# Performance work log

Hardware: AMD Instinct MI355X
Metric: run time of the kernel (lower is better)

## Reference

```python
import jax, jax.numpy as jnp
import numpy as np

HID, H, P = 1024, 16, 50  # hid_dim, n_heads, max_relative_position
DH = HID // H


def _rel_idx(len_q, len_k):
    # [Lq, Lk] clipped relative-distance indices into the (2P+1)-row table
    d = jnp.arange(len_k)[None, :] - jnp.arange(len_q)[:, None]
    return jnp.clip(d, -P, P) + P


def setup_inputs() -> dict:
    key = jax.random.key(0)
    ks = jax.random.split(key, 13)
    L, B = 2048, 2
    s = 0.02
    return {
        "query": jax.random.normal(ks[0], (L, B, HID), jnp.float32),
        "key": jax.random.normal(ks[1], (L, B, HID), jnp.float32),
        "value": jax.random.normal(ks[2], (L, B, HID), jnp.float32),
        "Wq": jax.random.normal(ks[3], (HID, HID), jnp.float32) * s,
        "bq": jax.random.normal(ks[4], (HID,), jnp.float32) * s,
        "Wk": jax.random.normal(ks[5], (HID, HID), jnp.float32) * s,
        "bk": jax.random.normal(ks[6], (HID,), jnp.float32) * s,
        "Wv": jax.random.normal(ks[7], (HID, HID), jnp.float32) * s,
        "bv": jax.random.normal(ks[8], (HID,), jnp.float32) * s,
        "Wo": jax.random.normal(ks[9], (HID, HID), jnp.float32) * s,
        "bo": jax.random.normal(ks[10], (HID,), jnp.float32) * s,
        "rel_k": jax.random.normal(ks[11], (2 * P + 1, DH), jnp.float32) * s,
        "rel_v": jax.random.normal(ks[12], (2 * P + 1, DH), jnp.float32) * s,
    }


def reference(query, key, value, Wq, bq, Wk, bk, Wv, bv, Wo, bo, rel_k, rel_v):
    # inputs are seq-first [L, B, hid]; torch code transposes to batch-first
    q = jnp.swapaxes(query, 0, 1)  # [B, Lq, hid]
    k = jnp.swapaxes(key, 0, 1)
    v = jnp.swapaxes(value, 0, 1)
    B, Lq, _ = q.shape
    Lk = k.shape[1]

    q = q @ Wq.T + bq
    k = k @ Wk.T + bk
    v = v @ Wv.T + bv

    # split heads: [B, H, L, DH]
    qh = q.reshape(B, Lq, H, DH).transpose(0, 2, 1, 3)
    kh = k.reshape(B, Lk, H, DH).transpose(0, 2, 1, 3)
    vh = v.reshape(B, Lk, H, DH).transpose(0, 2, 1, 3)

    idx = _rel_idx(Lq, Lk)
    Rk = rel_k[idx]  # [Lq, Lk, DH]
    Rv = rel_v[idx]  # [Lq, Lk, DH]

    attn1 = jnp.einsum('bhqd,bhkd->bhqk', qh, kh)
    attn2 = jnp.einsum('bhqd,qkd->bhqk', qh, Rk)
    scale = jnp.asarray(np.sqrt(DH), qh.dtype)
    attn = jax.nn.softmax((attn1 + attn2) / scale, axis=-1)  # dropout p=0 -> identity

    w1 = jnp.einsum('bhqk,bhkd->bhqd', attn, vh)
    w2 = jnp.einsum('bhqk,qkd->bhqd', attn, Rv)
    x = (w1 + w2).transpose(0, 2, 1, 3).reshape(B, Lq, HID)
    x = x @ Wo.T + bo
    return jnp.swapaxes(x, 0, 1)  # [Lq, B, hid]
```

## Files before the change

kernel.cpp:

```cpp
#include <hip/hip_runtime.h>


#define LSEQ 2048
#define HIDDIM 1024
#define NH 16
#define DHD 64
#define NREL 101
#define PMAX 50
#define SCL 0.18033688011112042f

typedef __attribute__((ext_vector_type(8))) __bf16 bf16x8;
typedef __attribute__((ext_vector_type(4))) float f32x4;

__device__ __forceinline__ unsigned short f2bf(float f) {
  unsigned int u = __builtin_bit_cast(unsigned int, f);
  u += 0x7fffu + ((u >> 16) & 1u);
  return (unsigned short)(u >> 16);
}
__device__ __forceinline__ float bflo(unsigned int u) { return __builtin_bit_cast(float, u << 16); }

__device__ __forceinline__ uint4 pack8(float4 f0, float4 f1) {
  uint4 o;
  o.x = (unsigned)f2bf(f0.x) | ((unsigned)f2bf(f0.y) << 16);
  o.y = (unsigned)f2bf(f0.z) | ((unsigned)f2bf(f0.w) << 16);
  o.z = (unsigned)f2bf(f1.x) | ((unsigned)f2bf(f1.y) << 16);
  o.w = (unsigned)f2bf(f1.z) | ((unsigned)f2bf(f1.w) << 16);
  return o;
}

__global__ void cast_w4(const float* __restrict__ s0, const float* __restrict__ s1,
                        const float* __restrict__ s2, const float* __restrict__ s3,
                        unsigned short* __restrict__ dst) {
  const int e = (blockIdx.x * 256 + threadIdx.x) * 8;
  const int g = e >> 20;
  const float* s = (g == 0) ? s0 : (g == 1) ? s1 : (g == 2) ? s2 : s3;
  const int o = e & 0xFFFFF;
  const float4 f0 = *(const float4*)(s + o);
  const float4 f1 = *(const float4*)(s + o + 4);
  *(uint4*)(dst + e) = pack8(f0, f1);
}

__global__ void cast_x_kernel(const float* __restrict__ src, unsigned short* __restrict__ dst) {
  const int e = (blockIdx.x * 256 + threadIdx.x) * 8;
  const int m = e >> 10, k = e & 1023;
  const int b = m >> 11, l = m & 2047;
  const float* s = src + (size_t)((l << 1) + b) * HIDDIM + k;
  const float4 f0 = *(const float4*)s;
  const float4 f1 = *(const float4*)(s + 4);
  *(uint4*)(dst + e) = pack8(f0, f1);
}

__global__ void cast_rk_kernel(const float* __restrict__ src, unsigned short* __restrict__ dst) {
  const int e = blockIdx.x * 256 + threadIdx.x;
  if (e >= 112 * 64) return;
  dst[e] = (e < NREL * 64) ? f2bf(src[e]) : (unsigned short)0;
}

__global__ void cast_rv_kernel(const float* __restrict__ src, unsigned short* __restrict__ dst) {
  const int e = blockIdx.x * 256 + threadIdx.x;
  if (e >= 64 * 128) return;
  const int d = e >> 7, j = e & 127;
  dst[e] = (j < NREL) ? f2bf(src[j * DHD + d]) : (unsigned short)0;
}

template <int MODE>
__global__ __launch_bounds__(256, 4) void gemm64(
    const unsigned short* __restrict__ A,
    const unsigned short* __restrict__ W,
    const float* __restrict__ bias,
    float* __restrict__ outF,
    unsigned short* __restrict__ outB) {
  constexpr int K = 1024;
  __shared__ unsigned short As[64 * 72];
  __shared__ unsigned short Bs[64 * 72];
  const int tid = threadIdx.x;
  const int tm = blockIdx.x >> 4, tn = blockIdx.x & 15;
  const int m0 = tm * 64, n0 = tn * 64;
  const int lane = tid & 63, wave = tid >> 6;
  const int wm = (wave >> 1) * 32, wn = (wave & 1) * 32;
  const int qr = lane & 15, quad = lane >> 4;
  const int sr = tid >> 3, sc = (tid & 7) * 8;
  f32x4 acc[2][2] = {};
  for (int k0 = 0; k0 < K; k0 += 64) {
    *(uint4*)&As[sr * 72 + sc]        = *(const uint4*)&A[(size_t)(m0 + sr) * K + k0 + sc];
    *(uint4*)&As[(sr + 32) * 72 + sc] = *(const uint4*)&A[(size_t)(m0 + sr + 32) * K + k0 + sc];
    *(uint4*)&Bs[sr * 72 + sc]        = *(const uint4*)&W[(size_t)(n0 + sr) * K + k0 + sc];
    *(uint4*)&Bs[(sr + 32) * 72 + sc] = *(const uint4*)&W[(size_t)(n0 + sr + 32) * K + k0 + sc];
    __syncthreads();
#pragma unroll
    for (int ks = 0; ks < 64; ks += 32) {
      bf16x8 a0 = *(const bf16x8*)&As[(wm + qr) * 72 + ks + quad * 8];
      bf16x8 a1 = *(const bf16x8*)&As[(wm + 16 + qr) * 72 + ks + quad * 8];
      bf16x8 b0 = *(const bf16x8*)&Bs[(wn + qr) * 72 + ks + quad * 8];
      bf16x8 b1 = *(const bf16x8*)&Bs[(wn + 16 + qr) * 72 + ks + quad * 8];
      acc[0][0] = __builtin_amdgcn_mfma_f32_16x16x32_bf16(a0, b0, acc[0][0], 0, 0, 0);
      acc[0][1] = __builtin_amdgcn_mfma_f32_16x16x32_bf16(a0, b1, acc[0][1], 0, 0, 0);
      acc[1][0] = __builtin_amdgcn_mfma_f32_16x16x32_bf16(a1, b0, acc[1][0], 0, 0, 0);
      acc[1][1] = __builtin_amdgcn_mfma_f32_16x16x32_bf16(a1, b1, acc[1][1], 0, 0, 0);
    }
    __syncthreads();
  }
#pragma unroll
  for (int i = 0; i < 2; i++)
#pragma unroll
    for (int j = 0; j < 2; j++) {
      const int n = n0 + wn + 16 * j + qr;
      const float bv = bias[n];
#pragma unroll
      for (int rr = 0; rr < 4; rr++) {
        const int m = m0 + wm + 16 * i + quad * 4 + rr;
        const float v = acc[i][j][rr] + bv;
        const int b = m >> 11, l = m & 2047;
        if (MODE == 0) {
          const int h = n >> 6, d = n & 63;
          outB[((size_t)((b * NH + h) * LSEQ + l) << 6) + d] = f2bf(v);
        } else if (MODE == 1) {
          outF[(size_t)((l << 1) + b) * HIDDIM + n] = v;
        } else {
          const int h = n >> 6, d = n & 63;
          outB[(size_t)((b * NH + h) * 64 + d) * LSEQ + l] = f2bf(v);
        }
      }
    }
}

#define KT 32
__global__ __launch_bounds__(256, 4) void attn_mfma(
    const unsigned short* __restrict__ Qb,
    const unsigned short* __restrict__ Kb,
    const unsigned short* __restrict__ Vgt,
    const unsigned short* __restrict__ RKb,
    const unsigned short* __restrict__ RVb,
    unsigned short* __restrict__ outB) {
  __shared__ __align__(16) unsigned short SH[20416];
  unsigned short* Kst = SH;
  unsigned short* Tb  = SH + 7424;
  unsigned short* SrS = SH + 13952;

  const int tid = threadIdx.x;
  const int xcd = blockIdx.x & 7, slot = blockIdx.x >> 3;
  const int bh = (slot >> 5) * 8 + xcd;
  const int q0 = (slot & 31) * 64;

  const int lane = tid & 63, wq = tid >> 6;
  const int c = lane & 15, quad = lane >> 4;
  const size_t base = (size_t)bh * (LSEQ * DHD);
  const unsigned short* Qp = Qb + base;
  const unsigned short* Kp = Kb + base;
  const unsigned short* Vp = Vgt + base;
  unsigned short* Ptw = SH + 4608 + wq * 704;

  const int qrow_w = q0 + wq * 16;
  const int srow = quad * 4;
  const int wrow0 = wq * 16 + srow;

  {
    unsigned* tz = (unsigned*)(Tb + wq * 1632);
    for (int e = lane; e < 816; e += 64) tz[e] = 0u;
  }

  const bf16x8 aq0 = *(const bf16x8*)&Qp[(size_t)(qrow_w + c) * DHD + quad * 8];
  const bf16x8 aq1 = *(const bf16x8*)&Qp[(size_t)(qrow_w + c) * DHD + 32 + quad * 8];

#pragma unroll
  for (int jt = 0; jt < 7; jt++) {
    bf16x8 b0 = *(const bf16x8*)&RKb[(jt * 16 + c) * DHD + quad * 8];
    bf16x8 b1 = *(const bf16x8*)&RKb[(jt * 16 + c) * DHD + 32 + quad * 8];
    f32x4 s4 = {};
    s4 = __builtin_amdgcn_mfma_f32_16x16x32_bf16(aq0, b0, s4, 0, 0, 0);
    s4 = __builtin_amdgcn_mfma_f32_16x16x32_bf16(aq1, b1, s4, 0, 0, 0);
    const int jc = jt * 16 + c;
    if (jc < NREL) {
#pragma unroll
      for (int r = 0; r < 4; r++) SrS[(wrow0 + r) * NREL + jc] = f2bf(s4[r]);
    }
  }

  float Srlo[4], Srhi[4];
#pragma unroll
  for (int r = 0; r < 4; r++) {
    Srlo[r] = bflo((unsigned)SrS[(wrow0 + r) * NREL + 0]);
    Srhi[r] = bflo((unsigned)SrS[(wrow0 + r) * NREL + 100]);
  }

  float rsum[4] = {0.f, 0.f, 0.f, 0.f};
  float lows[4] = {0.f, 0.f, 0.f, 0.f}, highs[4] = {0.f, 0.f, 0.f, 0.f};
  f32x4 Od[4] = {};

  const int strow = tid >> 3, stcol = (tid & 7) * 8;

  {
    uint4 k0r = *(const uint4*)&Kp[(size_t)strow * DHD + stcol];
    *(uint4*)&Kst[strow * 72 + stcol] = k0r;
  }
  __syncthreads();

  for (int it = 0; it < 64; ++it) {
    const int k0 = it * KT;
    const int cur = (it & 1) * 2304;
    uint4 kreg;
    if (it < 63) kreg = *(const uint4*)&Kp[(size_t)(k0 + KT + strow) * DHD + stcol];
    bf16x8 vf[4];
#pragma unroll
    for (int t = 0; t < 4; t++)
      vf[t] = *(const bf16x8*)&Vp[(size_t)(t * 16 + c) * LSEQ + k0 + quad * 8];

    const bf16x8 bk00 = *(const bf16x8*)&Kst[cur + c * 72 + quad * 8];
    const bf16x8 bk01 = *(const bf16x8*)&Kst[cur + c * 72 + 32 + quad * 8];
    const bf16x8 bk10 = *(const bf16x8*)&Kst[cur + (16 + c) * 72 + quad * 8];
    const bf16x8 bk11 = *(const bf16x8*)&Kst[cur + (16 + c) * 72 + 32 + quad * 8];
    f32x4 s0 = {}, s1 = {};
    s0 = __builtin_amdgcn_mfma_f32_16x16x32_bf16(aq0, bk00, s0, 0, 0, 0);
    s0 = __builtin_amdgcn_mfma_f32_16x16x32_bf16(aq1, bk01, s0, 0, 0, 0);
    s1 = __builtin_amdgcn_mfma_f32_16x16x32_bf16(aq0, bk10, s1, 0, 0, 0);
    s1 = __builtin_amdgcn_mfma_f32_16x16x32_bf16(aq1, bk11, s1, 0, 0, 0);

    const int mode = (k0 + KT - 1 <= qrow_w - 50) ? 0 : (k0 >= qrow_w + 65) ? 2 : 1;

#pragma unroll
    for (int kt = 0; kt < 2; kt++) {
      const f32x4 s = kt ? s1 : s0;
      const int kcol = k0 + kt * 16 + c;
#pragma unroll
      for (int r = 0; r < 4; r++) {
        float srv;
        int j = -1;
        if (mode == 0) srv = Srlo[r];
        else if (mode == 2) srv = Srhi[r];
        else {
          int dl = kcol - (qrow_w + srow + r);
          dl = dl < -PMAX ? -PMAX : (dl > PMAX ? PMAX : dl);
          j = dl + PMAX;
          srv = bflo((unsigned)SrS[(wrow0 + r) * NREL + j]);
        }
        const float p = exp2f((s[r] + srv) * SCL);
        const unsigned short pb = f2bf(p);
        const float pf = bflo((unsigned)pb);
        rsum[r] += pf;
        if (mode == 0) lows[r] += pf;
        else if (mode == 2) highs[r] += pf;
        else {
          if (j == 0) lows[r] += pf;
          else if (j == 100) highs[r] += pf;
          else Tb[(wrow0 + r) * 102 + j] = pb;
        }
        Ptw[(srow + r) * 44 + kt * 16 + c] = pb;
      }
    }

    const uint2 aplo = *(const uint2*)&Ptw[c * 44 + quad * 8];
    const uint2 aphi = *(const uint2*)&Ptw[c * 44 + quad * 8 + 4];
    const bf16x8 ap = __builtin_bit_cast(bf16x8, (uint4){aplo.x, aplo.y, aphi.x, aphi.y});
#pragma unroll
    for (int t = 0; t < 4; t++)
      Od[t] = __builtin_amdgcn_mfma_f32_16x16x32_bf16(ap, vf[t], Od[t], 0, 0, 0);

    if (it < 63) *(uint4*)&Kst[(cur ^ 2304) + strow * 72 + stcol] = kreg;
    __syncthreads();
  }

#pragma unroll
  for (int m = 1; m < 16; m <<= 1) {
#pragma unroll
    for (int r = 0; r < 4; r++) {
      rsum[r] += __shfl_xor(rsum[r], m, 64);
      lows[r] += __shfl_xor(lows[r], m, 64);
      highs[r] += __shfl_xor(highs[r], m, 64);
    }
  }
  if (c == 0) {
#pragma unroll
    for (int r = 0; r < 4; r++) {
      Tb[(wrow0 + r) * 102 + 0]   = f2bf(lows[r]);
      Tb[(wrow0 + r) * 102 + 100] = f2bf(highs[r]);
    }
  }
  __syncthreads();

#pragma unroll
  for (int kc = 0; kc < 4; kc++) {
    unsigned short a8[8];
#pragma unroll
    for (int jj = 0; jj < 8; jj++) {
      const int j = kc * 32 + quad * 8 + jj;
      a8[jj] = (j <= 100) ? Tb[(wq * 16 + c) * 102 + j] : (unsigned short)0;
    }
    bf16x8 at;
#pragma unroll
    for (int jj = 0; jj < 8; jj++) at[jj] = __builtin_bit_cast(__bf16, a8[jj]);
#pragma unroll
    for (int t = 0; t < 4; t++) {
      const bf16x8 bv = *(const bf16x8*)&RVb[(t * 16 + c) * 128 + kc * 32 + quad * 8];
      Od[t] = __builtin_amdgcn_mfma_f32_16x16x32_bf16(at, bv, Od[t], 0, 0, 0);
    }
  }

  const int b = bh >> 4, h = bh & 15;
#pragma unroll
  for (int r = 0; r < 4; r++) {
    const float inv = 1.f / rsum[r];
    const int qg = q0 + wq * 16 + srow + r;
    unsigned short* op = outB + (size_t)(b * LSEQ + qg) * HIDDIM + h * DHD + c;
#pragma unroll
    for (int t = 0; t < 4; t++) op[t * 16] = f2bf(Od[t][r] * inv);
  }
}

extern "C" void kernel_launch(void* const* d_in, const int* in_sizes, int n_in,
                              void* d_out, int out_size, void* d_ws, size_t ws_size,
                              hipStream_t stream) {
  const float* query = (const float*)d_in[0];
  const float* key   = (const float*)d_in[1];
  const float* value = (const float*)d_in[2];
  const float* Wq = (const float*)d_in[3];  const float* bq = (const float*)d_in[4];
  const float* Wk = (const float*)d_in[5];  const float* bk = (const float*)d_in[6];
  const float* Wv = (const float*)d_in[7];  const float* bv = (const float*)d_in[8];
  const float* Wo = (const float*)d_in[9];  const float* bo = (const float*)d_in[10];
  const float* relk = (const float*)d_in[11];
  const float* relv = (const float*)d_in[12];
  float* out = (float*)d_out;

  char* w = (char*)d_ws;
  const size_t MB = 1ull << 20;
  unsigned short* Wqb = (unsigned short*)(w + 0 * MB);
  unsigned short* Wkb = (unsigned short*)(w + 2 * MB);
  unsigned short* Wvb = (unsigned short*)(w + 4 * MB);
  unsigned short* Wob = (unsigned short*)(w + 6 * MB);
  unsigned short* Xb  = (unsigned short*)(w + 8 * MB);
  unsigned short* Qb  = (unsigned short*)(w + 16 * MB);
  unsigned short* Kb  = (unsigned short*)(w + 24 * MB);
  unsigned short* Vgt = (unsigned short*)(w + 32 * MB);
  unsigned short* AOb = Xb;
  unsigned short* RKb = Wqb;
  unsigned short* RVb = Wkb;

  cast_w4<<<2048, 256, 0, stream>>>(Wq, Wk, Wv, Wo, Wqb);

  cast_x_kernel<<<2048, 256, 0, stream>>>(query, Xb);
  gemm64<0><<<1024, 256, 0, stream>>>(Xb, Wqb, bq, nullptr, Qb);
  cast_rk_kernel<<<28, 256, 0, stream>>>(relk, RKb);
  cast_x_kernel<<<2048, 256, 0, stream>>>(key, Xb);
  gemm64<0><<<1024, 256, 0, stream>>>(Xb, Wkb, bk, nullptr, Kb);
  cast_rv_kernel<<<32, 256, 0, stream>>>(relv, RVb);
  cast_x_kernel<<<2048, 256, 0, stream>>>(value, Xb);
  gemm64<2><<<1024, 256, 0, stream>>>(Xb, Wvb, bv, nullptr, Vgt);

  attn_mfma<<<1024, 256, 0, stream>>>(Qb, Kb, Vgt, RKb, RVb, AOb);

  gemm64<1><<<1024, 256, 0, stream>>>(AOb, Wob, bo, out, nullptr);
}
```

Before: 390.5 us.

## Fuse QKV projections into one 128x128 GEMM with direct global-to-LDS loads

Replaces three separate cast-then-gemm64 sequences with a single cast kernel covering query/key/value and one batched QKV GEMM using 128x128 tiles, XOR-swizzled LDS, and global_load_lds transfers. The V output is transposed through shared memory so the Vgt stores are coalesced. The output buffer serves as scratch for the bf16 key and value inputs. This cuts launch count and redundant global traffic and raises per-block data reuse, at the cost of fewer blocks (768) and lower occupancy, plus a single-buffered load loop with no prefetch overlap.

```diff
diff --git a/kernel.cpp b/kernel.cpp
--- a/kernel.cpp
+++ b/kernel.cpp
@@ -12,6 +12,8 @@
 typedef __attribute__((ext_vector_type(8))) __bf16 bf16x8;
 typedef __attribute__((ext_vector_type(4))) float f32x4;
 
+#define MFMA(A, B, C) __builtin_amdgcn_mfma_f32_16x16x32_bf16(A, B, C, 0, 0, 0)
+
 __device__ __forceinline__ unsigned short f2bf(float f) {
   unsigned int u = __builtin_bit_cast(unsigned int, f);
   u += 0x7fffu + ((u >> 16) & 1u);
@@ -26,6 +28,12 @@
   o.z = (unsigned)f2bf(f1.x) | ((unsigned)f2bf(f1.y) << 16);
   o.w = (unsigned)f2bf(f1.z) | ((unsigned)f2bf(f1.w) << 16);
   return o;
+}
+
+__device__ __forceinline__ void gload16(const unsigned short* g, unsigned short* l) {
+  __builtin_amdgcn_global_load_lds(
+      (const __attribute__((address_space(1))) unsigned int*)g,
+      (__attribute__((address_space(3))) unsigned int*)l, 16, 0, 0);
 }
 
 __global__ void cast_w4(const float* __restrict__ s0, const float* __restrict__ s1,
@@ -40,13 +48,20 @@
   *(uint4*)(dst + e) = pack8(f0, f1);
 }
 
-__global__ void cast_x_kernel(const float* __restrict__ src, unsigned short* __restrict__ dst) {
-  const int e = (blockIdx.x * 256 + threadIdx.x) * 8;
-  const int m = e >> 10, k = e & 1023;
+__global__ void cast_x3(const float* __restrict__ q, const float* __restrict__ k,
+                        const float* __restrict__ v,
+                        unsigned short* __restrict__ dq, unsigned short* __restrict__ dk,
+                        unsigned short* __restrict__ dv) {
+  const int gid = blockIdx.x * 256 + threadIdx.x;
+  const int segi = gid >> 19;
+  const int e = (gid & 0x7FFFF) * 8;
+  const float* s = (segi == 0) ? q : (segi == 1) ? k : v;
+  unsigned short* dst = (segi == 0) ? dq : (segi == 1) ? dk : dv;
+  const int m = e >> 10, kk = e & 1023;
   const int b = m >> 11, l = m & 2047;
-  const float* s = src + (size_t)((l << 1) + b) * HIDDIM + k;
-  const float4 f0 = *(const float4*)s;
-  const float4 f1 = *(const float4*)(s + 4);
+  const float* sp = s + (size_t)((l << 1) + b) * HIDDIM + kk;
+  const float4 f0 = *(const float4*)sp;
+  const float4 f1 = *(const float4*)(sp + 4);
   *(uint4*)(dst + e) = pack8(f0, f1);
 }
 
@@ -61,6 +76,106 @@
   if (e >= 64 * 128) return;
   const int d = e >> 7, j = e & 127;
   dst[e] = (j < NREL) ? f2bf(src[j * DHD + d]) : (unsigned short)0;
+}
+
+__global__ __launch_bounds__(256, 3) void gemm_qkv(
+    const unsigned short* __restrict__ Xq, const unsigned short* __restrict__ Xk,
+    const unsigned short* __restrict__ Xv, const unsigned short* __restrict__ Wcat,
+    const float* __restrict__ bq, const float* __restrict__ bk, const float* __restrict__ bv,
+    unsigned short* __restrict__ Qb, unsigned short* __restrict__ Kb,
+    unsigned short* __restrict__ Vgt) {
+  __shared__ __align__(16) unsigned short SH[17408];
+  unsigned short* LA = SH;
+  unsigned short* LB = SH + 8192;
+
+  const int tid = threadIdx.x;
+  const int seg = blockIdx.x >> 8;
+  const int t = blockIdx.x & 255;
+  const int m0 = (t >> 3) * 128, n0 = (t & 7) * 128;
+
+  const unsigned short* A = (seg == 0) ? Xq : (seg == 1) ? Xk : Xv;
+  const unsigned short* W = Wcat + ((size_t)seg << 20);
+  const float* bias = (seg == 0) ? bq : (seg == 1) ? bk : bv;
+
+  const int lane = tid & 63, w = tid >> 6;
+  const int c = lane & 15, quad = lane >> 4;
+
+  const int srow = w * 32 + (lane >> 3);
+  const int scol = ((lane & 7) ^ (lane >> 3)) << 3;
+  const unsigned short* pA = A + (size_t)(m0 + srow) * 1024 + scol;
+  const unsigned short* pW = W + (size_t)(n0 + srow) * 1024 + scol;
+  unsigned short* lA = LA + w * 2048;
+  unsigned short* lB = LB + w * 2048;
+
+  const int wr = w >> 1, wc = w & 1;
+  const int cx = (c & 7) << 3;
+
+  f32x4 acc[4][4] = {};
+
+  for (int k0 = 0; k0 < 1024; k0 += 64) {
+#pragma unroll
+    for (int i = 0; i < 4; i++) {
+      gload16(pA + k0 + i * 8192, lA + i * 512);
+      gload16(pW + k0 + i * 8192, lB + i * 512);
+    }
+    __syncthreads();
+#pragma unroll
+    for (int ks = 0; ks < 2; ks++) {
+      bf16x8 af[4], bfr[4];
+#pragma unroll
+      for (int f = 0; f < 4; f++) {
+        af[f]  = *(const bf16x8*)&LA[(wr * 64 + f * 16 + c) * 64 + ((ks * 32 + quad * 8) ^ cx)];
+        bfr[f] = *(const bf16x8*)&LB[(wc * 64 + f * 16 + c) * 64 + ((ks * 32 + quad * 8) ^ cx)];
+      }
+#pragma unroll
+      for (int i = 0; i < 4; i++)
+#pragma unroll
+        for (int j = 0; j < 4; j++)
+          acc[i][j] = MFMA(af[i], bfr[j], acc[i][j]);
+    }
+    __syncthreads();
+  }
+
+  const int b = m0 >> 11, l0 = m0 & 2047;
+  const int h0 = n0 >> 6;
+  if (seg < 2) {
+    unsigned short* out = seg ? Kb : Qb;
+#pragma unroll
+    for (int i = 0; i < 4; i++)
+#pragma unroll
+      for (int j = 0; j < 4; j++) {
+        const int nl = wc * 64 + j * 16 + c;
+        const float bv_ = bias[n0 + nl];
+        const int h = h0 + (nl >> 6), d = nl & 63;
+#pragma unroll
+        for (int r = 0; r < 4; r++) {
+          const int l = l0 + wr * 64 + i * 16 + quad * 4 + r;
+          out[((size_t)((b * NH + h) * LSEQ + l) << 6) + d] = f2bf(acc[i][j][r] + bv_);
+        }
+      }
+  } else {
+    unsigned short* Ct = SH;
+#pragma unroll
+    for (int i = 0; i < 4; i++)
+#pragma unroll
+      for (int j = 0; j < 4; j++) {
+        const int nl = wc * 64 + j * 16 + c;
+        const float bv_ = bias[n0 + nl];
+#pragma unroll
+        for (int r = 0; r < 4; r++) {
+          const int ml = wr * 64 + i * 16 + quad * 4 + r;
+          Ct[nl * 136 + ml] = f2bf(acc[i][j][r] + bv_);
+        }
+      }
+    __syncthreads();
+    const int dr = tid >> 1, lc = (tid & 1) * 64;
+    const int h = h0 + (dr >> 6), dd = dr & 63;
+    unsigned short* dst = Vgt + ((size_t)((b * NH + h) * 64 + dd)) * LSEQ + l0 + lc;
+    const unsigned short* src = Ct + dr * 136 + lc;
+#pragma unroll
+    for (int u = 0; u < 8; u++)
+      *(uint4*)(dst + u * 8) = *(const uint4*)(src + u * 8);
+  }
 }
 
 template <int MODE>
@@ -93,10 +208,10 @@
       bf16x8 a1 = *(const bf16x8*)&As[(wm + 16 + qr) * 72 + ks + quad * 8];
       bf16x8 b0 = *(const bf16x8*)&Bs[(wn + qr) * 72 + ks + quad * 8];
       bf16x8 b1 = *(const bf16x8*)&Bs[(wn + 16 + qr) * 72 + ks + quad * 8];
-      acc[0][0] = __builtin_amdgcn_mfma_f32_16x16x32_bf16(a0, b0, acc[0][0], 0, 0, 0);
-      acc[0][1] = __builtin_amdgcn_mfma_f32_16x16x32_bf16(a0, b1, acc[0][1], 0, 0, 0);
-      acc[1][0] = __builtin_amdgcn_mfma_f32_16x16x32_bf16(a1, b0, acc[1][0], 0, 0, 0);
-      acc[1][1] = __builtin_amdgcn_mfma_f32_16x16x32_bf16(a1, b1, acc[1][1], 0, 0, 0);
+      acc[0][0] = MFMA(a0, b0, acc[0][0]);
+      acc[0][1] = MFMA(a0, b1, acc[0][1]);
+      acc[1][0] = MFMA(a1, b0, acc[1][0]);
+      acc[1][1] = MFMA(a1, b1, acc[1][1]);
     }
     __syncthreads();
   }
@@ -111,14 +226,8 @@
         const int m = m0 + wm + 16 * i + quad * 4 + rr;
         const float v = acc[i][j][rr] + bv;
         const int b = m >> 11, l = m & 2047;
-        if (MODE == 0) {
-          const int h = n >> 6, d = n & 63;
-          outB[((size_t)((b * NH + h) * LSEQ + l) << 6) + d] = f2bf(v);
-        } else if (MODE == 1) {
+        if (MODE == 1) {
           outF[(size_t)((l << 1) + b) * HIDDIM + n] = v;
-        } else {
-          const int h = n >> 6, d = n & 63;
-          outB[(size_t)((b * NH + h) * 64 + d) * LSEQ + l] = f2bf(v);
         }
       }
     }
@@ -167,8 +276,8 @@
     bf16x8 b0 = *(const bf16x8*)&RKb[(jt * 16 + c) * DHD + quad * 8];
     bf16x8 b1 = *(const bf16x8*)&RKb[(jt * 16 + c) * DHD + 32 + quad * 8];
     f32x4 s4 = {};
-    s4 = __builtin_amdgcn_mfma_f32_16x16x32_bf16(aq0, b0, s4, 0, 0, 0);
-    s4 = __builtin_amdgcn_mfma_f32_16x16x32_bf16(aq1, b1, s4, 0, 0, 0);
+    s4 = MFMA(aq0, b0, s4);
+    s4 = MFMA(aq1, b1, s4);
     const int jc = jt * 16 + c;
     if (jc < NREL) {
 #pragma unroll
@@ -210,10 +319,10 @@
     const bf16x8 bk10 = *(const bf16x8*)&Kst[cur + (16 + c) * 72 + quad * 8];
     const bf16x8 bk11 = *(const bf16x8*)&Kst[cur + (16 + c) * 72 + 32 + quad * 8];
     f32x4 s0 = {}, s1 = {};
-    s0 = __builtin_amdgcn_mfma_f32_16x16x32_bf16(aq0, bk00, s0, 0, 0, 0);
-    s0 = __builtin_amdgcn_mfma_f32_16x16x32_bf16(aq1, bk01, s0, 0, 0, 0);
-    s1 = __builtin_amdgcn_mfma_f32_16x16x32_bf16(aq0, bk10, s1, 0, 0, 0);
-    s1 = __builtin_amdgcn_mfma_f32_16x16x32_bf16(aq1, bk11, s1, 0, 0, 0);
+    s0 = MFMA(aq0, bk00, s0);
+    s0 = MFMA(aq1, bk01, s0);
+    s1 = MFMA(aq0, bk10, s1);
+    s1 = MFMA(aq1, bk11, s1);
 
     const int mode = (k0 + KT - 1 <= qrow_w - 50) ? 0 : (k0 >= qrow_w + 65) ? 2 : 1;
 
@@ -253,7 +362,7 @@
     const bf16x8 ap = __builtin_bit_cast(bf16x8, (uint4){aplo.x, aplo.y, aphi.x, aphi.y});
 #pragma unroll
     for (int t = 0; t < 4; t++)
-      Od[t] = __builtin_amdgcn_mfma_f32_16x16x32_bf16(ap, vf[t], Od[t], 0, 0, 0);
+      Od[t] = MFMA(ap, vf[t], Od[t]);
 
     if (it < 63) *(uint4*)&Kst[(cur ^ 2304) + strow * 72 + stcol] = kreg;
     __syncthreads();
@@ -291,7 +400,7 @@
 #pragma unroll
     for (int t = 0; t < 4; t++) {
       const bf16x8 bv = *(const bf16x8*)&RVb[(t * 16 + c) * 128 + kc * 32 + quad * 8];
-      Od[t] = __builtin_amdgcn_mfma_f32_16x16x32_bf16(at, bv, Od[t], 0, 0, 0);
+      Od[t] = MFMA(at, bv, Od[t]);
     }
   }
 
@@ -322,30 +431,23 @@
 
   char* w = (char*)d_ws;
   const size_t MB = 1ull << 20;
-  unsigned short* Wqb = (unsigned short*)(w + 0 * MB);
-  unsigned short* Wkb = (unsigned short*)(w + 2 * MB);
-  unsigned short* Wvb = (unsigned short*)(w + 4 * MB);
-  unsigned short* Wob = (unsigned short*)(w + 6 * MB);
-  unsigned short* Xb  = (unsigned short*)(w + 8 * MB);
-  unsigned short* Qb  = (unsigned short*)(w + 16 * MB);
-  unsigned short* Kb  = (unsigned short*)(w + 24 * MB);
-  unsigned short* Vgt = (unsigned short*)(w + 32 * MB);
-  unsigned short* AOb = Xb;
-  unsigned short* RKb = Wqb;
-  unsigned short* RVb = Wkb;
-
-  cast_w4<<<2048, 256, 0, stream>>>(Wq, Wk, Wv, Wo, Wqb);
-
-  cast_x_kernel<<<2048, 256, 0, stream>>>(query, Xb);
-  gemm64<0><<<1024, 256, 0, stream>>>(Xb, Wqb, bq, nullptr, Qb);
+  unsigned short* Wcat = (unsigned short*)(w + 0 * MB);
+  unsigned short* Wob  = (unsigned short*)(w + 6 * MB);
+  unsigned short* Xq   = (unsigned short*)(w + 8 * MB);
+  unsigned short* Qb   = (unsigned short*)(w + 16 * MB);
+  unsigned short* Kb   = (unsigned short*)(w + 24 * MB);
+  unsigned short* Vgt  = (unsigned short*)(w + 32 * MB);
+  unsigned short* AOb  = Xq;
+  unsigned short* RKb  = Wcat;
+  unsigned short* RVb  = (unsigned short*)(w + 2 * MB);
+  unsigned short* Xk = (unsigned short*)out;
+  unsigned short* Xv = (unsigned short*)out + (4u << 20);
+
+  cast_w4<<<2048, 256, 0, stream>>>(Wq, Wk, Wv, Wo, Wcat);
+  cast_x3<<<6144, 256, 0, stream>>>(query, key, value, Xq, Xk, Xv);
+  gemm_qkv<<<768, 256, 0, stream>>>(Xq, Xk, Xv, Wcat, bq, bk, bv, Qb, Kb, Vgt);
   cast_rk_kernel<<<28, 256, 0, stream>>>(relk, RKb);
-  cast_x_kernel<<<2048, 256, 0, stream>>>(key, Xb);
-  gemm64<0><<<1024, 256, 0, stream>>>(Xb, Wkb, bk, nullptr, Kb);
   cast_rv_kernel<<<32, 256, 0, stream>>>(relv, RVb);
-  cast_x_kernel<<<2048, 256, 0, stream>>>(value, Xb);
-  gemm64<2><<<1024, 256, 0, stream>>>(Xb, Wvb, bv, nullptr, Vgt);
-
   attn_mfma<<<1024, 256, 0, stream>>>(Qb, Kb, Vgt, RKb, RVb, AOb);
-
   gemm64<1><<<1024, 256, 0, stream>>>(AOb, Wob, bo, out, nullptr);
 }
```

Measured after the change: 334.8 us. 1.17x faster.
